# Performance work log

Hardware: AMD Instinct MI355X
Metric: run time of the kernel (lower is better)

## Reference

```python
import jax, jax.numpy as jnp
import numpy as np

B, S, D, H = 2, 2048, 2048, 16
HD = D // H  # head_dim = 128

def _rope_tables(head_dim, context_length, theta_base=10000.0):
    inv_freq = 1.0 / theta_base ** (jnp.arange(0, head_dim, 2, dtype=jnp.float32) / head_dim)
    pos = jnp.arange(context_length, dtype=jnp.float32)
    angles = pos[:, None] * inv_freq[None, :]            # [S, HD/2]
    angles = jnp.concatenate([angles, angles], axis=1)   # [S, HD]
    return jnp.cos(angles), jnp.sin(angles)

def _apply_rope(x, cos, sin):
    # x: [b, h, s, hd]; cos/sin: [s, hd]
    hd = x.shape[-1]
    x1, x2 = x[..., : hd // 2], x[..., hd // 2 :]
    rotated = jnp.concatenate([-x2, x1], axis=-1)
    return x * cos[None, None] + rotated * sin[None, None]

def setup_inputs() -> dict:
    key = jax.random.key(0)
    ks = jax.random.split(key, 5)
    x = jax.random.normal(ks[0], (B, S, D), dtype=jnp.float32)
    scale = 1.0 / np.sqrt(D)
    Wq = jax.random.normal(ks[1], (D, D), dtype=jnp.float32) * scale
    Wk = jax.random.normal(ks[2], (D, D), dtype=jnp.float32) * scale
    Wv = jax.random.normal(ks[3], (D, D), dtype=jnp.float32) * scale
    Wo = jax.random.normal(ks[4], (D, D), dtype=jnp.float32) * scale
    cos, sin = _rope_tables(HD, S)
    return {"x": x, "Wq": Wq, "Wk": Wk, "Wv": Wv, "Wo": Wo, "cos": cos, "sin": sin}

def reference(x, Wq, Wk, Wv, Wo, cos, sin):
    b, s, _ = x.shape
    def split_heads(t):  # [b,s,D] -> [b,H,s,HD]
        return t.reshape(b, s, H, HD).transpose(0, 2, 1, 3)
    q = split_heads(x @ Wq.T)
    k = split_heads(x @ Wk.T)
    v = split_heads(x @ Wv.T)
    q = _apply_rope(q, cos[:s], sin[:s])
    k = _apply_rope(k, cos[:s], sin[:s])
    scores = jnp.einsum("bhqd,bhkd->bhqk", q, k) / np.sqrt(HD)
    causal = jnp.triu(jnp.ones((s, s), dtype=bool), k=1)
    scores = jnp.where(causal[None, None], -jnp.inf, scores)
    weights = jax.nn.softmax(scores, axis=-1)
    ctx = jnp.einsum("bhqk,bhkd->bhqd", weights, v)
    ctx = ctx.transpose(0, 2, 1, 3).reshape(b, s, D)
    return ctx @ Wo.T
```

## Files before the change

### kernel.cpp

```cpp
#include <hip/hip_runtime.h>
#include <cstdint>
#include <cmath>

#define B_ 2
#define S_ 2048
#define D_ 2048
#define H_ 16
#define HD_ 128

#define NEG_SENTINEL -1.0e30f

typedef __bf16 bf16;
typedef __attribute__((ext_vector_type(4))) __bf16 bf16x4;
typedef __attribute__((ext_vector_type(8))) __bf16 bf16x8;
typedef __attribute__((ext_vector_type(4))) float f32x4;

__device__ __forceinline__ void gload_lds16(const void* g, void* l) {
  __builtin_amdgcn_global_load_lds(
      (const __attribute__((address_space(1))) unsigned int*)g,
      (__attribute__((address_space(3))) unsigned int*)l, 16, 0, 0);
}

__device__ __forceinline__ f32x4 mfma16(bf16x8 a, bf16x8 b, f32x4 c) {
  return __builtin_amdgcn_mfma_f32_16x16x32_bf16(a, b, c, 0, 0, 0);
}

__device__ __forceinline__ void wg_barrier() {
  asm volatile("" ::: "memory");
  __builtin_amdgcn_s_barrier();
  asm volatile("" ::: "memory");
}

__global__ __launch_bounds__(256) void cvt_f32_bf16(
    const float* __restrict__ in, bf16* __restrict__ out)
{
  int i = blockIdx.x * 256 + threadIdx.x;
  f32x4 v = ((const f32x4*)in)[i];
  bf16x4 o;
#pragma unroll
  for (int j = 0; j < 4; ++j) o[j] = (bf16)v[j];
  ((bf16x4*)out)[i] = o;
}

#define GTM 128
#define GTN 128
#define GBK 64

template <typename OT>
__global__ __launch_bounds__(256) void gemm_xwt(
    const bf16* __restrict__ A, const bf16* __restrict__ W, OT* __restrict__ C,
    int M, int N, int K, int ldc)
{
  __shared__ bf16 sA[GTM * GBK];
  __shared__ bf16 sB[GTN * GBK];
  const int tid  = threadIdx.x;
  const int wave = tid >> 6, lane = tid & 63;
  const int quad = lane >> 4, l16 = lane & 15;
  const int tm = blockIdx.y * GTM;
  const int tn = blockIdx.x * GTN;
  const int wm = (wave >> 1) * 64, wn = (wave & 1) * 64;

  f32x4 acc[4][4];
#pragma unroll
  for (int i = 0; i < 4; ++i)
#pragma unroll
    for (int j = 0; j < 4; ++j) acc[i][j] = (f32x4)0.0f;

  for (int k0 = 0; k0 < K; k0 += GBK) {
    __syncthreads();
#pragma unroll
    for (int g = 0; g < 4; ++g) {
      int gb  = (g * 4 + wave) * 64;
      int p   = gb + lane;
      int row = p >> 3, pos = p & 7;
      int cc  = pos ^ (row & 7);
      gload_lds16(A + (size_t)(tm + row) * K + k0 + cc * 8, (char*)sA + (size_t)gb * 16);
      gload_lds16(W + (size_t)(tn + row) * K + k0 + cc * 8, (char*)sB + (size_t)gb * 16);
    }
    __syncthreads();

#pragma unroll
    for (int t = 0; t < 2; ++t) {
      bf16x8 af[4], bfr[4];
#pragma unroll
      for (int i = 0; i < 4; ++i) {
        int rowa = wm + i * 16 + l16;
        int posa = (t * 4 + quad) ^ (rowa & 7);
        af[i] = *(const bf16x8*)(sA + rowa * GBK + posa * 8);
        int rowb = wn + i * 16 + l16;
        int posb = (t * 4 + quad) ^ (rowb & 7);
        bfr[i] = *(const bf16x8*)(sB + rowb * GBK + posb * 8);
      }
#pragma unroll
      for (int i = 0; i < 4; ++i)
#pragma unroll
        for (int j = 0; j < 4; ++j)
          acc[i][j] = mfma16(af[i], bfr[j], acc[i][j]);
    }
  }

#pragma unroll
  for (int i = 0; i < 4; ++i)
#pragma unroll
    for (int r = 0; r < 4; ++r) {
      int row = tm + wm + i * 16 + quad * 4 + r;
#pragma unroll
      for (int j = 0; j < 4; ++j) {
        int col = tn + wn + j * 16 + l16;
        C[(size_t)row * ldc + col] = (OT)acc[i][j][r];
      }
    }
}

#define PTM 256
#define PTN 128
#define PBK 64
#define PBUFB 49152
#define PLDSB 98304

#define STAGE_AU(kt_, u_) do { \
    char* dstA_ = smem + (((kt_) & 1) * PBUFB); \
    _Pragma("unroll") \
    for (int g2_ = 0; g2_ < 2; ++g2_) { \
      int row0_ = (u_) * 64 + g2_ * 128 + wave * 8; \
      int row_  = row0_ + (lane >> 3); \
      int cc_   = (lane & 7) ^ (row_ & 7); \
      gload_lds16(A + (size_t)(tm + row_) * K + (size_t)(kt_) * PBK + cc_ * 8, \
                  dstA_ + row0_ * 128); \
    } } while (0)

#define STAGE_BF(kt_) do { \
    char* dstB_ = smem + (((kt_) & 1) * PBUFB) + 32768; \
    _Pragma("unroll") \
    for (int g2_ = 0; g2_ < 2; ++g2_) { \
      int row0_ = g2_ * 64 + wave * 8; \
      int row_  = row0_ + (lane >> 3); \
      int cc_   = (lane & 7) ^ (row_ & 7); \
      gload_lds16(W + (size_t)(tn + row_) * K + (size_t)(kt_) * PBK + cc_ * 8, \
                  dstB_ + row0_ * 128); \
    } } while (0)

template <typename OT>
__global__ __launch_bounds__(512, 2) void gemm_pipe(
    const bf16* __restrict__ A, const bf16* __restrict__ W, OT* __restrict__ C,
    int M, int N, int K, int ldc, int nby)
{
  extern __shared__ char smem[];
  const int tid  = threadIdx.x;
  const int wave = tid >> 6, lane = tid & 63;
  const int quad = lane >> 4, l16 = lane & 15;

  const int nwg = (int)gridDim.x;
  const int cpx = nwg >> 3;
  const int wg  = ((int)blockIdx.x & 7) * cpx + ((int)blockIdx.x >> 3);
  const int bx = wg / nby, by = wg % nby;
  const int tm = by * PTM, tn = bx * PTN;
  const int wm = (wave >> 2) * 128, wn = (wave & 3) * 32;

  const int NT = K / PBK;

  f32x4 acc[8][2];
#pragma unroll
  for (int i = 0; i < 8; ++i)
#pragma unroll
    for (int j = 0; j < 2; ++j) acc[i][j] = (f32x4)0.0f;

  STAGE_AU(0, 0);
  STAGE_AU(0, 1);
  STAGE_BF(0);
  if (NT > 1) STAGE_AU(1, 0);
  asm volatile("s_waitcnt vmcnt(2)" ::: "memory");
  wg_barrier();

#pragma unroll 1
  for (int t = 0; t < NT; ++t) {
    const bf16* sAb = (const bf16*)(smem + (t & 1) * PBUFB);
    const bf16* sBb = sAb + 16384;
    bf16x8 a[4][2], b[2][2];

#pragma unroll
    for (int i = 0; i < 4; ++i)
#pragma unroll
      for (int t2 = 0; t2 < 2; ++t2) {
        int r  = wm + i * 16 + l16;
        int ps = (t2 * 4 + quad) ^ (r & 7);
        a[i][t2] = *(const bf16x8*)(sAb + r * 64 + ps * 8);
      }
#pragma unroll
    for (int j = 0; j < 2; ++j)
#pragma unroll
      for (int t2 = 0; t2 < 2; ++t2) {
        int r  = wn + j * 16 + l16;
        int ps = (t2 * 4 + quad) ^ (r & 7);
        b[j][t2] = *(const bf16x8*)(sBb + r * 64 + ps * 8);
      }
    if (t + 1 < NT) { STAGE_AU(t + 1, 1); STAGE_BF(t + 1); }
    wg_barrier();
    __builtin_amdgcn_s_setprio(1);
#pragma unroll
    for (int i = 0; i < 4; ++i)
#pragma unroll
      for (int j = 0; j < 2; ++j)
#pragma unroll
        for (int t2 = 0; t2 < 2; ++t2)
          acc[i][j] = mfma16(a[i][t2], b[j][t2], acc[i][j]);
    __builtin_amdgcn_s_setprio(0);
    wg_barrier();

#pragma unroll
    for (int i = 0; i < 4; ++i)
#pragma unroll
      for (int t2 = 0; t2 < 2; ++t2) {
        int r  = wm + 64 + i * 16 + l16;
        int ps = (t2 * 4 + quad) ^ (r & 7);
        a[i][t2] = *(const bf16x8*)(sAb + r * 64 + ps * 8);
      }
    if (t + 2 < NT) STAGE_AU(t + 2, 0);
    wg_barrier();
    __builtin_amdgcn_s_setprio(1);
#pragma unroll
    for (int i = 0; i < 4; ++i)
#pragma unroll
      for (int j = 0; j < 2; ++j)
#pragma unroll
        for (int t2 = 0; t2 < 2; ++t2)
          acc[4 + i][j] = mfma16(a[i][t2], b[j][t2], acc[4 + i][j]);
    __builtin_amdgcn_s_setprio(0);
    if (t + 2 >= NT) { asm volatile("s_waitcnt vmcnt(0)" ::: "memory"); }
    else             { asm volatile("s_waitcnt vmcnt(2)" ::: "memory"); }
    wg_barrier();
  }

#pragma unroll
  for (int i = 0; i < 8; ++i)
#pragma unroll
    for (int r = 0; r < 4; ++r) {
      int row = tm + wm + i * 16 + quad * 4 + r;
#pragma unroll
      for (int j = 0; j < 2; ++j) {
        int col = tn + wn + j * 16 + l16;
        C[(size_t)row * ldc + col] = (OT)acc[i][j][r];
      }
    }
}

__global__ __launch_bounds__(256) void rope_qk(
    bf16* __restrict__ Q, bf16* __restrict__ Kk,
    const float* __restrict__ cosT, const float* __restrict__ sinT, int rs)
{
  const float kappa = 0.08838834764831845f * 1.4426950408889634f;
  int t = blockIdx.x * 256 + threadIdx.x;
  int d = t & 63;
  int h = (t >> 6) & (H_ - 1);
  int s = (t >> 10) & (S_ - 1);
  int b = t >> 21;
  size_t base = ((size_t)(b * S_ + s)) * rs + (size_t)h * HD_;
  float c1 = cosT[s * HD_ + d];
  float s1 = sinT[s * HD_ + d];
  float c2 = cosT[s * HD_ + d + 64];
  float s2 = sinT[s * HD_ + d + 64];
  {
    float x1 = (float)Q[base + d], x2 = (float)Q[base + d + 64];
    Q[base + d]      = (bf16)((x1 * c1 - x2 * s1) * kappa);
    Q[base + d + 64] = (bf16)((x2 * c2 + x1 * s2) * kappa);
  }
  {
    float x1 = (float)Kk[base + d], x2 = (float)Kk[base + d + 64];
    Kk[base + d]      = (bf16)(x1 * c1 - x2 * s1);
    Kk[base + d + 64] = (bf16)(x2 * c2 + x1 * s2);
  }
}

__global__ __launch_bounds__(256) void transpose_v(
    const bf16* __restrict__ V, bf16* __restrict__ Vt, int rs)
{
  __shared__ bf16 sT[64 * 72];
  const int tid = threadIdx.x;
  const int si = blockIdx.x;
  const int di = blockIdx.y;
  const int bh = blockIdx.z;
  const int b  = bh >> 4, h = bh & 15;

  const bf16* src = V + (size_t)b * S_ * rs + (size_t)h * HD_ + di * 64;
  bf16*       dst = Vt + ((size_t)bh * HD_ + di * 64) * S_ + si * 64;

#pragma unroll
  for (int half = 0; half < 2; ++half) {
    int r  = half * 32 + (tid >> 3);
    int c0 = (tid & 7) * 8;
    bf16x8 v = *(const bf16x8*)(src + (size_t)(si * 64 + r) * rs + c0);
    *(bf16x8*)(sT + r * 72 + c0) = v;
  }
  __syncthreads();
#pragma unroll
  for (int half = 0; half < 2; ++half) {
    int dr = half * 32 + (tid >> 3);
    int c0 = (tid & 7) * 8;
    bf16x8 o;
#pragma unroll
    for (int j = 0; j < 8; ++j) o[j] = sT[(c0 + j) * 72 + dr];
    *(bf16x8*)(dst + (size_t)dr * S_ + c0) = o;
  }
}

#define ABK 64
#define SPS 72

__global__ __launch_bounds__(256) void attn_fwd(
    const bf16* __restrict__ Q, const bf16* __restrict__ K,
    const bf16* __restrict__ Vt, bf16* __restrict__ O, int rs)
{
  __shared__ bf16 sK[ABK * HD_];
  __shared__ bf16 sVT[HD_ * ABK];
  __shared__ bf16 sP[64 * SPS];

  const int tid  = threadIdx.x;
  const int wave = tid >> 6, lane = tid & 63;
  const int quad = lane >> 4, l16 = lane & 15;

  const int lin   = (int)blockIdx.x;
  const int low3  = lin & 7;
  const int rest  = lin >> 3;
  const int pairx = rest & 15;
  const int colhi = rest >> 4;
  const int col   = low3 + (colhi << 3);
  const int b = col >> 4, h = col & 15;

  const bf16* Qh  = Q + (size_t)b * S_ * rs + (size_t)h * HD_;
  const bf16* Kh  = K + (size_t)b * S_ * rs + (size_t)h * HD_;
  const bf16* Vth = Vt + ((size_t)(b * H_ + h) * HD_) * S_;
  bf16*       Oh  = O + (size_t)b * S_ * D_ + (size_t)h * HD_;

  const int wq = wave * 16;

#pragma unroll 1
  for (int seg = 0; seg < 2; ++seg) {
    const int qt = seg == 0 ? pairx : 31 - pairx;
    const int q0 = qt * 64;
    const int wq_abs = q0 + wq;

    bf16x8 qf[4];
    {
      const bf16* rp = Qh + (size_t)(wq_abs + l16) * rs + quad * 8;
#pragma unroll
      for (int t = 0; t < 4; ++t) qf[t] = *(const bf16x8*)(rp + t * 32);
    }

    f32x4 o_acc[8];
#pragma unroll
    for (int j = 0; j < 8; ++j) o_acc[j] = (f32x4)0.0f;
    float m_col = NEG_SENTINEL;
    float l_col = 0.0f;

    const int nkt = qt + 1;
#pragma unroll 1
    for (int kt = 0; kt < nkt; ++kt) {
      const int kk0 = kt * ABK;
      __syncthreads();

#pragma unroll
      for (int g = 0; g < 4; ++g) {
        int p   = g * 256 + tid;
        int row = p >> 4, pos = p & 15;
        int cc  = pos ^ (row & 15);
        gload_lds16(Kh + (size_t)(kk0 + row) * rs + cc * 8, (char*)sK + (size_t)p * 16);
      }
#pragma unroll
      for (int g = 0; g < 4; ++g) {
        int p  = g * 256 + tid;
        int d  = p >> 3, pos = p & 7;
        int cc = pos ^ (d & 7);
        gload_lds16(Vth + (size_t)d * S_ + kk0 + cc * 8, (char*)sVT + (size_t)p * 16);
      }
      __syncthreads();

      if (kk0 <= wq_abs + 15) {
        f32x4 st[4];
#pragma unroll
        for (int jt = 0; jt < 4; ++jt) {
          bf16x8 kf[4];
#pragma unroll
          for (int t = 0; t < 4; ++t) {
            int pos = (t * 4 + quad) ^ l16;
            kf[t] = *(const bf16x8*)(sK + (jt * 16 + l16) * HD_ + pos * 8);
          }
          f32x4 a = (f32x4)0.0f;
#pragma unroll
          for (int t = 0; t < 4; ++t) a = mfma16(kf[t], qf[t], a);
          st[jt] = a;
        }

        if (kk0 + 63 > wq_abs) {
          int qcol = wq_abs + l16;
#pragma unroll
          for (int jt = 0; jt < 4; ++jt)
#pragma unroll
            for (int r = 0; r < 4; ++r) {
              int key = kk0 + jt * 16 + quad * 4 + r;
              if (key > qcol) st[jt][r] = NEG_SENTINEL;
            }
        }

        float mx = NEG_SENTINEL;
#pragma unroll
        for (int jt = 0; jt < 4; ++jt)
#pragma unroll
          for (int r = 0; r < 4; ++r) mx = fmaxf(mx, st[jt][r]);
        mx = fmaxf(mx, __shfl_xor(mx, 16, 64));
        mx = fmaxf(mx, __shfl_xor(mx, 32, 64));
        float m_new = fmaxf(m_col, mx);
        float alpha = exp2f(m_col - m_new);
        float ts = 0.0f;
#pragma unroll
        for (int jt = 0; jt < 4; ++jt) {
          bf16x4 pk;
#pragma unroll
          for (int r = 0; r < 4; ++r) {
            float p = exp2f(st[jt][r] - m_new);
            ts += p;
            pk[r] = (bf16)p;
          }
          *(bf16x4*)(sP + (wq + l16) * SPS + jt * 16 + quad * 4) = pk;
        }
        ts += __shfl_xor(ts, 16, 64);
        ts += __shfl_xor(ts, 32, 64);
        l_col = l_col * alpha + ts;
        m_col = m_new;
#pragma unroll
        for (int r = 0; r < 4; ++r) {
          float av = __shfl(alpha, quad * 4 + r, 64);
#pragma unroll
          for (int jd = 0; jd < 8; ++jd) o_acc[jd][r] *= av;
        }

#pragma unroll
        for (int ks = 0; ks < 2; ++ks) {
          bf16x8 pf = *(const bf16x8*)(sP + (wq + l16) * SPS + ks * 32 + quad * 8);
#pragma unroll
          for (int jd = 0; jd < 8; ++jd) {
            int pos = (ks * 4 + quad) ^ (l16 & 7);
            bf16x8 vf = *(const bf16x8*)(sVT + (jd * 16 + l16) * ABK + pos * 8);
            o_acc[jd] = mfma16(pf, vf, o_acc[jd]);
          }
        }
      }
    }

#pragma unroll
    for (int r = 0; r < 4; ++r) {
      float lv = __shfl(l_col, quad * 4 + r, 64);
      float inv_l = 1.0f / lv;
      int row = wq_abs + quad * 4 + r;
#pragma unroll
      for (int jd = 0; jd < 8; ++jd) {
        int colo = jd * 16 + l16;
        Oh[(size_t)row * D_ + colo] = (bf16)(o_acc[jd][r] * inv_l);
      }
    }
  }
}

extern "C" void kernel_launch(void* const* d_in, const int* in_sizes, int n_in,
                              void* d_out, int out_size, void* d_ws, size_t ws_size,
                              hipStream_t stream) {
  const float* x    = (const float*)d_in[0];
  const float* Wq   = (const float*)d_in[1];
  const float* Wk   = (const float*)d_in[2];
  const float* Wv   = (const float*)d_in[3];
  const float* Wo   = (const float*)d_in[4];
  const float* cosT = (const float*)d_in[5];
  const float* sinT = (const float*)d_in[6];
  float* out = (float*)d_out;

  const size_t NE = (size_t)B_ * S_ * D_;
  const size_t WE = (size_t)D_ * D_;
  const int M = B_ * S_;
  const int cvtX = (int)(NE / 1024);
  const int cvtW = (int)(WE / 1024);

  static bool attr_done = false;
  if (!attr_done) {
    (void)hipFuncSetAttribute(reinterpret_cast<const void*>(gemm_pipe<bf16>),
                              hipFuncAttributeMaxDynamicSharedMemorySize, PLDSB);
    (void)hipFuncSetAttribute(reinterpret_cast<const void*>(gemm_pipe<float>),
                              hipFuncAttributeMaxDynamicSharedMemorySize, PLDSB);
    attr_done = true;
  }

  if (ws_size >= (size_t)92274688) {
    bf16* QKV   = (bf16*)d_ws;
    bf16* xb    = QKV + (size_t)M * 6144;
    bf16* Wqkv  = xb + NE;
    bf16* ctx   = Wqkv;
    bf16* Wob   = Wqkv + 2 * WE;
    bf16* Vt    = xb;

    cvt_f32_bf16<<<cvtX, 256, 0, stream>>>(x, xb);
    cvt_f32_bf16<<<cvtW, 256, 0, stream>>>(Wq, Wqkv);
    cvt_f32_bf16<<<cvtW, 256, 0, stream>>>(Wk, Wqkv + WE);
    cvt_f32_bf16<<<cvtW, 256, 0, stream>>>(Wv, Wqkv + 2 * WE);
    gemm_pipe<bf16><<<768, 512, PLDSB, stream>>>(xb, Wqkv, QKV, M, 3 * D_, D_, 3 * D_, 16);
    rope_qk<<<(B_ * S_ * H_ * 64) / 256, 256, 0, stream>>>(QKV, QKV + D_, cosT, sinT, 3 * D_);
    transpose_v<<<dim3(32, 2, 32), 256, 0, stream>>>(QKV + 2 * D_, Vt, 3 * D_);
    attn_fwd<<<512, 256, 0, stream>>>(QKV, QKV + D_, Vt, ctx, 3 * D_);
    cvt_f32_bf16<<<cvtW, 256, 0, stream>>>(Wo, Wob);
    gemm_pipe<float><<<256, 512, PLDSB, stream>>>(ctx, Wob, out, M, D_, D_, D_, 16);
  } else {
    bf16* Qb    = (bf16*)d_ws;
    bf16* Kb    = Qb + NE;
    bf16* Vb    = Kb + NE;
    bf16* Cb    = Vb + NE;
    bf16* Wslot = Cb + NE;

    cvt_f32_bf16<<<cvtX, 256, 0, stream>>>(x, Cb);
    cvt_f32_bf16<<<cvtW, 256, 0, stream>>>(Wq, Wslot);
    gemm_xwt<bf16><<<dim3(16, 32), 256, 0, stream>>>(Cb, Wslot, Qb, M, D_, D_, D_);
    cvt_f32_bf16<<<cvtW, 256, 0, stream>>>(Wk, Wslot);
    gemm_xwt<bf16><<<dim3(16, 32), 256, 0, stream>>>(Cb, Wslot, Kb, M, D_, D_, D_);
    cvt_f32_bf16<<<cvtW, 256, 0, stream>>>(Wv, Wslot);
    gemm_xwt<bf16><<<dim3(16, 32), 256, 0, stream>>>(Cb, Wslot, Vb, M, D_, D_, D_);
    rope_qk<<<(B_ * S_ * H_ * 64) / 256, 256, 0, stream>>>(Qb, Kb, cosT, sinT, D_);
    transpose_v<<<dim3(32, 2, 32), 256, 0, stream>>>(Vb, Cb, D_);
    attn_fwd<<<512, 256, 0, stream>>>(Qb, Kb, Cb, Vb, D_);
    cvt_f32_bf16<<<cvtW, 256, 0, stream>>>(Wo, Wslot);
    gemm_xwt<float><<<dim3(16, 32), 256, 0, stream>>>(Vb, Wslot, out, M, D_, D_, D_);
  }
}
```

Baseline: 410.3 us.

## Triple-buffer LDS in pipelined GEMM to prefetch two k-tiles ahead

Converts the gemm_pipe LDS staging from a double buffer with partial-tile lookahead into a three-slot ring buffer. Loads for tile t+2 are issued while tile t is computed, and the vmcnt waits are relaxed accordingly. The goal is to hide more global-load latency behind MFMA work. In exchange, LDS use grows to 144KB per workgroup, which with launch_bounds(512,2) may cut occupancy to one workgroup per CU, or the kernel may fail to launch if the dynamic shared size isn't updated.

```diff
diff --git a/kernel.cpp b/kernel.cpp
--- a/kernel.cpp
+++ b/kernel.cpp
@@ -116,10 +116,10 @@
 #define PTN 128
 #define PBK 64
 #define PBUFB 49152
-#define PLDSB 98304
-
-#define STAGE_AU(kt_, u_) do { \
-    char* dstA_ = smem + (((kt_) & 1) * PBUFB); \
+#define PLDSB 147456
+
+#define STAGE_AU(kt_, u_, bi_) do { \
+    char* dstA_ = smem + ((bi_) * PBUFB); \
     _Pragma("unroll") \
     for (int g2_ = 0; g2_ < 2; ++g2_) { \
       int row0_ = (u_) * 64 + g2_ * 128 + wave * 8; \
@@ -129,8 +129,8 @@
                   dstA_ + row0_ * 128); \
     } } while (0)
 
-#define STAGE_BF(kt_) do { \
-    char* dstB_ = smem + (((kt_) & 1) * PBUFB) + 32768; \
+#define STAGE_BF(kt_, bi_) do { \
+    char* dstB_ = smem + ((bi_) * PBUFB) + 32768; \
     _Pragma("unroll") \
     for (int g2_ = 0; g2_ < 2; ++g2_) { \
       int row0_ = g2_ * 64 + wave * 8; \
@@ -165,17 +165,25 @@
 #pragma unroll
     for (int j = 0; j < 2; ++j) acc[i][j] = (f32x4)0.0f;
 
-  STAGE_AU(0, 0);
-  STAGE_AU(0, 1);
-  STAGE_BF(0);
-  if (NT > 1) STAGE_AU(1, 0);
-  asm volatile("s_waitcnt vmcnt(2)" ::: "memory");
+  STAGE_AU(0, 0, 0);
+  STAGE_AU(0, 1, 0);
+  STAGE_BF(0, 0);
+  if (NT > 1) {
+    STAGE_AU(1, 0, 1);
+    STAGE_AU(1, 1, 1);
+    STAGE_BF(1, 1);
+    asm volatile("s_waitcnt vmcnt(6)" ::: "memory");
+  } else {
+    asm volatile("s_waitcnt vmcnt(0)" ::: "memory");
+  }
   wg_barrier();
 
+  int bi = 0;
 #pragma unroll 1
   for (int t = 0; t < NT; ++t) {
-    const bf16* sAb = (const bf16*)(smem + (t & 1) * PBUFB);
+    const bf16* sAb = (const bf16*)(smem + bi * PBUFB);
     const bf16* sBb = sAb + 16384;
+    int bi2 = bi + 2; if (bi2 >= 3) bi2 -= 3;
     bf16x8 a[4][2], b[2][2];
 
 #pragma unroll
@@ -194,7 +202,7 @@
         int ps = (t2 * 4 + quad) ^ (r & 7);
         b[j][t2] = *(const bf16x8*)(sBb + r * 64 + ps * 8);
       }
-    if (t + 1 < NT) { STAGE_AU(t + 1, 1); STAGE_BF(t + 1); }
+    if (t + 2 < NT) { STAGE_AU(t + 2, 0, bi2); STAGE_AU(t + 2, 1, bi2); }
     wg_barrier();
     __builtin_amdgcn_s_setprio(1);
 #pragma unroll
@@ -215,7 +223,7 @@
         int ps = (t2 * 4 + quad) ^ (r & 7);
         a[i][t2] = *(const bf16x8*)(sAb + r * 64 + ps * 8);
       }
-    if (t + 2 < NT) STAGE_AU(t + 2, 0);
+    if (t + 2 < NT) STAGE_BF(t + 2, bi2);
     wg_barrier();
     __builtin_amdgcn_s_setprio(1);
 #pragma unroll
@@ -227,8 +235,10 @@
           acc[4 + i][j] = mfma16(a[i][t2], b[j][t2], acc[4 + i][j]);
     __builtin_amdgcn_s_setprio(0);
     if (t + 2 >= NT) { asm volatile("s_waitcnt vmcnt(0)" ::: "memory"); }
-    else             { asm volatile("s_waitcnt vmcnt(2)" ::: "memory"); }
+    else             { asm volatile("s_waitcnt vmcnt(6)" ::: "memory"); }
     wg_barrier();
+
+    bi = bi + 1; if (bi >= 3) bi = 0;
   }
 
 #pragma unroll
```

Result: no change. 406.6 us (-0.9%).
